# Optimization experiments

Measured on AMD Instinct MI355X. Metric: run time of the kernel, lower is better.

## Reference

```python
import jax, jax.numpy as jnp
import numpy as np

N, IN_DIM, OUT_DIM, NUM_HOPS, SD = 8192, 256, 256, 4, 64
ETA, LAM_LAP, LAM_SP, EPS = 0.5, 0.3, 0.05, 0.5
LN_EPS = 1e-5


def setup_inputs() -> dict:
    key = jax.random.key(0)
    ks = jax.random.split(key, 6)
    K = NUM_HOPS + 1
    return {
        "H": jax.random.normal(ks[0], (N, IN_DIM), jnp.float32),
        "hops": jax.random.normal(ks[1], (K, N, IN_DIM), jnp.float32),
        "L": jax.random.normal(ks[2], (N, N), jnp.float32),
        "U": jax.random.normal(ks[3], (K, IN_DIM, SD), jnp.float32) * 0.1,
        "W_in": jax.random.normal(ks[4], (OUT_DIM, IN_DIM), jnp.float32) * 0.05,
        "ln_gamma": jnp.ones((OUT_DIM,), jnp.float32),
        "ln_beta": jnp.zeros((OUT_DIM,), jnp.float32),
        "log_tau": jnp.zeros((), jnp.float32),
    }


def _per_hop(U_k, H_k):
    n = H_k.shape[0]
    Q, _ = jnp.linalg.qr(U_k)                 # [in_dim, sd]
    Z = Q.T @ H_k.T                           # [sd, n]
    G = Z @ Z.T                               # [sd, sd] Gram, reused
    Sigma = G / (n + 1e-8)
    tr_S = jnp.trace(Sigma)
    tr_S2 = jnp.sum(Sigma * Sigma)            # trace(Sigma @ Sigma), Sigma symmetric
    rank_eff = tr_S ** 2 / (tr_S2 + 1e-8)
    coeff = SD / (n * EPS ** 2 + 1e-8)
    M = jnp.eye(SD, dtype=Z.dtype) + coeff * G
    Lc = jnp.linalg.cholesky(M)
    MiZ = jax.scipy.linalg.cho_solve((Lc, True), Z)  # [sd, n]
    grad_R = (Q @ MiZ).T                      # [n, in_dim]
    return rank_eff, grad_R


def reference(H, hops, L, U, W_in, ln_gamma, ln_beta, log_tau):
    tau = jnp.clip(jnp.exp(log_tau), 0.1, 10.0)
    rank_effs, grads_R = jax.vmap(_per_hop)(U, hops)      # [K], [K,n,in_dim]
    lap_terms = jnp.einsum('nm,kmd->knd', L, hops)        # [K,n,in_dim]
    w = jax.nn.softmax(rank_effs / tau)                   # [K]
    grad_sum = jnp.einsum('k,knd->nd', w, grads_R)
    lap_sum = jnp.einsum('k,knd->nd', w, lap_terms)
    H_half = H + ETA * grad_sum - ETA * LAM_LAP * lap_sum
    H_prox = jnp.sign(H_half) * jax.nn.relu(jnp.abs(H_half) - LAM_SP * ETA)
    H_out = H_prox @ W_in.T
    mu = jnp.mean(H_out, axis=-1, keepdims=True)
    var = jnp.var(H_out, axis=-1, keepdims=True)
    H_out = (H_out - mu) * jax.lax.rsqrt(var + LN_EPS) * ln_gamma + ln_beta
    return H_out, rank_effs, w
```

## Files before the change

### kernel.cpp

```cpp
#include <hip/hip_runtime.h>
#include <stdint.h>


typedef __attribute__((ext_vector_type(8))) short  s16x8;
typedef __attribute__((ext_vector_type(4))) float  f32x4;

#define NNODE 8192
#define DIN   256
#define KHOP  5
#define SDM   64

static const size_t OFF_Q    = 0;
static const size_t OFF_QT   = OFF_Q   + (size_t)5*256*64*4;
static const size_t OFF_ZT   = OFF_QT  + (size_t)5*64*256*2;
static const size_t OFF_GP   = OFF_ZT  + (size_t)5*8192*64*2;
static const size_t OFF_LM   = OFF_GP  + (size_t)5*16*4096*4;
static const size_t OFF_RD   = OFF_LM  + (size_t)5*4096*4;
static const size_t OFF_LU   = OFF_RD  + (size_t)5*64*4;
static const size_t OFF_RDU  = OFF_LU  + (size_t)5*4096*4;
static const size_t OFF_RE   = OFF_RDU + (size_t)5*64*4;
static const size_t OFF_W    = OFF_RE  + 64;
static const size_t OFF_T2   = OFF_W   + 64;
static const size_t OFF_HWT  = OFF_T2  + (size_t)5*256*64*2;
static const size_t OFF_WBF  = OFF_HWT + (size_t)256*8192*2;
static const size_t OFF_HP   = OFF_WBF + (size_t)256*256*2;
static const size_t OFF_PART = OFF_HP  + (size_t)8192*256*2;
static const size_t OFF_LBF  = OFF_PART + (size_t)9*8192*256*2;

__device__ __forceinline__ unsigned short f2bf(float f){
  unsigned u = __builtin_bit_cast(unsigned, f);
  u += 0x7FFFu + ((u >> 16) & 1u);
  return (unsigned short)(u >> 16);
}
__device__ __forceinline__ float bf2f(unsigned h){
  return __builtin_bit_cast(float, h << 16);
}
__device__ __forceinline__ void gl_lds16(const void* g, void* l){
  __builtin_amdgcn_global_load_lds(
      (const __attribute__((address_space(1))) void*)g,
      (__attribute__((address_space(3))) void*)l, 16, 0, 0);
}
__device__ __forceinline__ f32x4 mfma16(s16x8 a, s16x8 b, f32x4 c){
  return __builtin_amdgcn_mfma_f32_16x16x32_bf16(a, b, c, 0, 0, 0);
}

__device__ void chol64(float* A, float* rd, int tid){
  #pragma unroll 1
  for (int j = 0; j < 64; ++j){
    if (tid == 0){
      float d = sqrtf(fmaxf(A[j*65+j], 1e-20f));
      A[j*65+j] = d; rd[j] = 1.0f / d;
    }
    __syncthreads();
    float rinv = rd[j];
    for (int i = j+1+tid; i < 64; i += 256) A[i*65+j] *= rinv;
    __syncthreads();
    #pragma unroll 1
    for (int e = tid; e < 4096; e += 256){
      int i = e >> 6, l = e & 63;
      if (i > j && l > j && l <= i) A[i*65+l] -= A[i*65+j] * A[l*65+j];
    }
    __syncthreads();
  }
}

__global__ __launch_bounds__(256) void k_pre(const float* __restrict__ U,
                                             const float* __restrict__ L,
                                             float* __restrict__ Lu,
                                             float* __restrict__ rdu,
                                             unsigned short* __restrict__ Lbf){
  __shared__ float A[64*65];
  __shared__ float rd[64];
  int tid = threadIdx.x;
  if (blockIdx.x >= 5){
    size_t e = ((size_t)(blockIdx.x-5)*256 + tid)*8;
    f32x4 a = *(const f32x4*)(L + e);
    f32x4 b = *(const f32x4*)(L + e + 4);
    uint4 u;
    u.x = (unsigned)f2bf(a[0]) | ((unsigned)f2bf(a[1]) << 16);
    u.y = (unsigned)f2bf(a[2]) | ((unsigned)f2bf(a[3]) << 16);
    u.z = (unsigned)f2bf(b[0]) | ((unsigned)f2bf(b[1]) << 16);
    u.w = (unsigned)f2bf(b[2]) | ((unsigned)f2bf(b[3]) << 16);
    *(uint4*)(Lbf + e) = u;
    return;
  }
  int k = blockIdx.x;
  const float* Uk = U + (size_t)k*16384;
  int ti = tid >> 4, tj = tid & 15;
  float s[16];
  #pragma unroll
  for (int i = 0; i < 16; ++i) s[i] = 0.0f;
  for (int n = 0; n < 256; ++n){
    f32x4 xa = *(const f32x4*)(Uk + n*64 + ti*4);
    f32x4 xb = *(const f32x4*)(Uk + n*64 + tj*4);
    #pragma unroll
    for (int p = 0; p < 4; ++p)
      #pragma unroll
      for (int q = 0; q < 4; ++q) s[p*4+q] += xa[p]*xb[q];
  }
  #pragma unroll
  for (int p = 0; p < 4; ++p)
    #pragma unroll
    for (int q = 0; q < 4; ++q) A[(ti*4+p)*65 + tj*4+q] = s[p*4+q];
  __syncthreads();
  chol64(A, rd, tid);
  for (int e = tid; e < 4096; e += 256) Lu[(size_t)k*4096 + e] = A[(e>>6)*65 + (e&63)];
  if (tid < 64) rdu[k*64 + tid] = rd[tid];
}

__global__ __launch_bounds__(256) void k_qsolve(const float* __restrict__ U,
                                                const float* __restrict__ Lu,
                                                const float* __restrict__ rdu,
                                                float* __restrict__ Qf,
                                                unsigned short* __restrict__ Qt){
  int k = blockIdx.y, tid = threadIdx.x, wave = tid >> 6, lane = tid & 63;
  __shared__ float Al[64*65];
  __shared__ float rds[64];
  for (int e = tid; e < 4096; e += 256) Al[(e>>6)*65 + (e&63)] = Lu[(size_t)k*4096 + e];
  if (tid < 64) rds[tid] = rdu[k*64 + tid];
  __syncthreads();
  int n = blockIdx.x*4 + wave;
  float x = U[((size_t)k*256 + n)*64 + lane];
  #pragma unroll
  for (int j = 0; j < 64; ++j){
    float zj = __shfl(x, j) * rds[j];
    x = (lane == j) ? zj : (lane > j ? x - Al[lane*65+j]*zj : x);
  }
  Qf[((size_t)k*256 + n)*64 + lane] = x;
  Qt[(size_t)k*16384 + lane*256 + n] = f2bf(x);
}

__global__ __launch_bounds__(256,2) void k_zgemm(const float* __restrict__ hops,
                                                 const unsigned short* __restrict__ Qt,
                                                 unsigned short* __restrict__ Zt){
  __shared__ __align__(16) unsigned short Al[128][72];
  __shared__ __align__(16) unsigned short Bl[64][64];
  int tid = threadIdx.x, lane = tid & 63, wave = tid >> 6;
  int q = lane >> 4, r = lane & 15;
  int k = blockIdx.y, m0 = blockIdx.x * 128;
  f32x4 acc[2][4];
  #pragma unroll
  for (int a = 0; a < 2; ++a)
    #pragma unroll
    for (int b = 0; b < 4; ++b) acc[a][b] = (f32x4){0,0,0,0};
  int rr = tid >> 1, half = tid & 1;
  for (int it = 0; it < 4; ++it){
    __syncthreads();
    #pragma unroll
    for (int i = 0; i < 2; ++i){
      int o = i*4096 + wave*1024 + lane*16;
      int srow = o >> 7, kc = (o & 127) >> 1;
      gl_lds16(Qt + (size_t)k*16384 + srow*256 + it*64 + kc,
               (char*)&Bl[0][0] + i*4096 + wave*1024);
    }
    const float* ga = hops + ((size_t)k*NNODE + m0 + rr)*256 + it*64 + half*32;
    f32x4 v[8];
    #pragma unroll
    for (int i = 0; i < 8; ++i) v[i] = *(const f32x4*)(ga + i*4);
    #pragma unroll
    for (int i = 0; i < 4; ++i){
      s16x8 t;
      #pragma unroll
      for (int j = 0; j < 8; ++j){ int e = i*8+j; t[j] = (short)f2bf(v[e>>2][e&3]); }
      *(s16x8*)&Al[rr][half*32 + i*8] = t;
    }
    __syncthreads();
    #pragma unroll
    for (int h = 0; h < 2; ++h){
      int ko = h*32 + q*8;
      s16x8 b[4];
      #pragma unroll
      for (int ni = 0; ni < 4; ++ni) b[ni] = *(const s16x8*)&Bl[ni*16 + r][ko];
      #pragma unroll
      for (int mi = 0; mi < 2; ++mi){
        s16x8 a = *(const s16x8*)&Al[wave*32 + mi*16 + r][ko];
        #pragma unroll
        for (int ni = 0; ni < 4; ++ni) acc[mi][ni] = mfma16(a, b[ni], acc[mi][ni]);
      }
    }
  }
  #pragma unroll
  for (int mi = 0; mi < 2; ++mi)
    #pragma unroll
    for (int ni = 0; ni < 4; ++ni)
      #pragma unroll
      for (int ii = 0; ii < 4; ++ii){
        int m = m0 + wave*32 + mi*16 + q*4 + ii;
        int sc = ni*16 + r;
        Zt[((size_t)k*NNODE + m)*64 + sc] = f2bf(acc[mi][ni][ii]);
      }
}

__global__ __launch_bounds__(256) void k_gpart(const unsigned short* __restrict__ Zt,
                                               float* __restrict__ Gp){
  int k = blockIdx.x, c = blockIdx.y, tid = threadIdx.x;
  __shared__ __align__(16) unsigned short Zl[128][64];
  int ti = tid >> 4, tj = tid & 15;
  float acc[16];
  #pragma unroll
  for (int i = 0; i < 16; ++i) acc[i] = 0.0f;
  for (int sub = 0; sub < 4; ++sub){
    const char* gb = (const char*)Zt + ((size_t)k*NNODE + c*512 + sub*128)*128;
    __syncthreads();
    #pragma unroll
    for (int i = 0; i < 4; ++i){
      int o = i*4096 + tid*16;
      *(uint4*)((char*)&Zl[0][0] + o) = *(const uint4*)(gb + o);
    }
    __syncthreads();
    for (int n = 0; n < 128; ++n){
      const unsigned short* row = &Zl[n][0];
      uint2 ua = *(const uint2*)(row + ti*4);
      uint2 ub = *(const uint2*)(row + tj*4);
      float xa[4] = { bf2f(ua.x & 0xffff), bf2f(ua.x >> 16), bf2f(ua.y & 0xffff), bf2f(ua.y >> 16) };
      float xb[4] = { bf2f(ub.x & 0xffff), bf2f(ub.x >> 16), bf2f(ub.y & 0xffff), bf2f(ub.y >> 16) };
      #pragma unroll
      for (int p = 0; p < 4; ++p)
        #pragma unroll
        for (int qn = 0; qn < 4; ++qn) acc[p*4+qn] += xa[p]*xb[qn];
    }
  }
  float* o = Gp + ((size_t)k*16 + c)*4096;
  #pragma unroll
  for (int p = 0; p < 4; ++p)
    #pragma unroll
    for (int qn = 0; qn < 4; ++qn) o[(ti*4+p)*64 + tj*4+qn] = acc[p*4+qn];
}

__global__ __launch_bounds__(256) void k_gred(const float* __restrict__ Gp,
                                              float* __restrict__ LmO,
                                              float* __restrict__ rdO,
                                              float* __restrict__ reO){
  int k = blockIdx.x, tid = threadIdx.x;
  __shared__ float A[64*65];
  __shared__ float rd[64];
  __shared__ float red[256];
  int ti = tid >> 4, tj = tid & 15;
  float s[16];
  #pragma unroll
  for (int i = 0; i < 16; ++i) s[i] = 0.0f;
  for (int c = 0; c < 16; ++c){
    const float* g = Gp + ((size_t)k*16 + c)*4096 + (ti*4)*64 + tj*4;
    #pragma unroll
    for (int p = 0; p < 4; ++p)
      #pragma unroll
      for (int qn = 0; qn < 4; ++qn) s[p*4+qn] += g[p*64+qn];
  }
  const float sc    = 1.0f / (8192.0f + 1e-8f);
  const float coeff = 64.0f / (8192.0f*0.25f + 1e-8f);
  float trp = 0.0f, tr2p = 0.0f;
  #pragma unroll
  for (int p = 0; p < 4; ++p)
    #pragma unroll
    for (int qn = 0; qn < 4; ++qn){
      float gg = s[p*4+qn];
      float sg = gg * sc;
      tr2p += sg*sg;
      int row = ti*4+p, col = tj*4+qn;
      if (row == col) trp += sg;
      A[row*65 + col] = (row == col ? 1.0f : 0.0f) + coeff*gg;
    }
  red[tid] = trp; __syncthreads();
  for (int o = 128; o > 0; o >>= 1){ if (tid < o) red[tid] += red[tid+o]; __syncthreads(); }
  float tr = red[0]; __syncthreads();
  red[tid] = tr2p; __syncthreads();
  for (int o = 128; o > 0; o >>= 1){ if (tid < o) red[tid] += red[tid+o]; __syncthreads(); }
  float tr2 = red[0]; __syncthreads();
  if (tid == 0) reO[k] = tr*tr / (tr2 + 1e-8f);
  chol64(A, rd, tid);
  for (int e = tid; e < 4096; e += 256) LmO[(size_t)k*4096 + e] = A[(e>>6)*65 + (e&63)];
  if (tid < 64) rdO[k*64 + tid] = rd[tid];
}

__global__ void k_soft(const float* __restrict__ re, const float* __restrict__ ltau,
                       float* __restrict__ wv, float* __restrict__ dtail){
  if (threadIdx.x == 0){
    float tau = expf(ltau[0]);
    tau = fminf(fmaxf(tau, 0.1f), 10.0f);
    float r[5], m = -1e30f;
    for (int i = 0; i < 5; ++i){ r[i] = re[i]; m = fmaxf(m, r[i]); }
    float e[5], sum = 0.0f;
    for (int i = 0; i < 5; ++i){ e[i] = expf((r[i]-m)/tau); sum += e[i]; }
    for (int i = 0; i < 5; ++i){
      float w = e[i]/sum;
      wv[i] = w; dtail[i] = r[i]; dtail[5+i] = w;
    }
  }
}

__global__ __launch_bounds__(256) void k_post(const float* __restrict__ hops,
                                              const float* __restrict__ wv,
                                              unsigned short* __restrict__ hwT,
                                              const float* __restrict__ Qf,
                                              const float* __restrict__ LmI,
                                              const float* __restrict__ rdI,
                                              unsigned short* __restrict__ T2w,
                                              const float* __restrict__ Win,
                                              unsigned short* __restrict__ Wbf){
  __shared__ float T[64*65];
  __shared__ float rds[64];
  int bid = blockIdx.x, tid = threadIdx.x;
  if (bid < 512){
    int n0 = (bid & 127)*64, d0 = (bid >> 7)*64;
    float wl[5];
    #pragma unroll
    for (int k = 0; k < 5; ++k) wl[k] = -0.15f * wv[k];
    for (int e = tid; e < 1024; e += 256){
      int row = e >> 4, c4 = (e & 15)*4;
      f32x4 acc = (f32x4){0,0,0,0};
      #pragma unroll
      for (int k = 0; k < 5; ++k){
        f32x4 v = *(const f32x4*)(hops + ((size_t)k*NNODE + n0 + row)*256 + d0 + c4);
        acc += v * wl[k];
      }
      T[row*65 + c4+0] = acc[0]; T[row*65 + c4+1] = acc[1];
      T[row*65 + c4+2] = acc[2]; T[row*65 + c4+3] = acc[3];
    }
    __syncthreads();
    for (int e = tid; e < 1024; e += 256){
      int dr = e >> 4, c4 = (e & 15)*4;
      unsigned short h0 = f2bf(T[(c4+0)*65 + dr]);
      unsigned short h1 = f2bf(T[(c4+1)*65 + dr]);
      unsigned short h2 = f2bf(T[(c4+2)*65 + dr]);
      unsigned short h3 = f2bf(T[(c4+3)*65 + dr]);
      uint2 u; u.x = (unsigned)h0 | ((unsigned)h1 << 16); u.y = (unsigned)h2 | ((unsigned)h3 << 16);
      *(uint2*)(hwT + (size_t)(d0+dr)*NNODE + n0 + c4) = u;
    }
  } else if (bid < 832){
    int i = bid - 512;
    int k = i >> 6, xb = i & 63;
    int wave = tid >> 6, lane = tid & 63;
    for (int e = tid; e < 4096; e += 256) T[(e>>6)*65 + (e&63)] = LmI[(size_t)k*4096 + e];
    if (tid < 64) rds[tid] = rdI[k*64 + tid];
    __syncthreads();
    int n = xb*4 + wave;
    float x = Qf[((size_t)k*256 + n)*64 + lane];
    #pragma unroll
    for (int j = 0; j < 64; ++j){
      float zj = __shfl(x, j) * rds[j];
      x = (lane == j) ? zj : (lane > j ? x - T[lane*65+j]*zj : x);
    }
    #pragma unroll
    for (int j = 63; j >= 0; --j){
      float yj = __shfl(x, j) * rds[j];
      x = (lane == j) ? yj : (lane < j ? x - T[j*65+lane]*yj : x);
    }
    float scale = 0.5f * wv[k];
    T2w[((size_t)k*256 + n)*64 + lane] = f2bf(scale * x);
  } else {
    int i = bid - 832;
    int e = (i*256 + tid)*4;
    f32x4 v = *(const f32x4*)(Win + e);
    uint2 u;
    u.x = (unsigned)f2bf(v[0]) | ((unsigned)f2bf(v[1]) << 16);
    u.y = (unsigned)f2bf(v[2]) | ((unsigned)f2bf(v[3]) << 16);
    *(uint2*)(Wbf + e) = u;
  }
}

__global__ __launch_bounds__(256,2) void k_gg(const unsigned short* __restrict__ Lbf,
                                              const unsigned short* __restrict__ Bt,
                                              unsigned short* __restrict__ part,
                                              const unsigned short* __restrict__ Zt,
                                              const unsigned short* __restrict__ T2w){
  __shared__ __align__(16) unsigned short SM[24960];
  int bid = blockIdx.x, tid = threadIdx.x;
  int lane = tid & 63, wave = tid >> 6;
  int q = lane >> 4, r = lane & 15;
  if (bid < 512){
    unsigned short* Al = SM;
    unsigned short* Bl = SM + 16*520;
    int m0 = (bid & 63) * 128;
    int by = bid >> 6;
    size_t kbase = (size_t)by * 1024;
    int sr = lane >> 3, sc8 = (lane & 7) * 8;
    f32x4 acc[8][4];
    #pragma unroll
    for (int a = 0; a < 8; ++a)
      #pragma unroll
      for (int b = 0; b < 4; ++b) acc[a][b] = (f32x4){0,0,0,0};
    for (int it = 0; it < 16; ++it){
      size_t k0 = kbase + it*64;
      __syncthreads();
      #pragma unroll
      for (int i = 0; i < 12; ++i){
        int c = i*4 + wave;
        if (c < 16){
          gl_lds16(Lbf + (size_t)(m0 + c*8 + sr)*NNODE + k0 + sc8,
                   (char*)Al + c*1040 + lane*16);
        } else {
          int cb = c - 16;
          gl_lds16(Bt + (size_t)(cb*8 + sr)*NNODE + k0 + sc8,
                   (char*)Bl + cb*1040 + lane*16);
        }
      }
      __syncthreads();
      #pragma unroll
      for (int h = 0; h < 2; ++h){
        int ko = h*32 + q*8;
        s16x8 b[4];
        #pragma unroll
        for (int ni = 0; ni < 4; ++ni){
          int d = wave*64 + ni*16 + r;
          b[ni] = *(const s16x8*)(Bl + (d>>3)*520 + (d&7)*64 + ko);
        }
        #pragma unroll
        for (int mi = 0; mi < 8; ++mi){
          int m = mi*16 + r;
          s16x8 a = *(const s16x8*)(Al + (m>>3)*520 + (m&7)*64 + ko);
          #pragma unroll
          for (int ni = 0; ni < 4; ++ni) acc[mi][ni] = mfma16(a, b[ni], acc[mi][ni]);
        }
      }
    }
    unsigned short* o = part + (size_t)by * 2097152;
    #pragma unroll
    for (int mi = 0; mi < 8; ++mi)
      #pragma unroll
      for (int ni = 0; ni < 4; ++ni)
        #pragma unroll
        for (int ii = 0; ii < 4; ++ii){
          int m = m0 + mi*16 + q*4 + ii;
          int n = wave*64 + ni*16 + r;
          o[(size_t)m*256 + n] = f2bf(acc[mi][ni][ii]);
        }
  } else {
    unsigned short* Al = SM;
    unsigned short* Bl = SM + 2048;
    int m0 = (bid - 512) * 32;
    f32x4 acc[2][4];
    #pragma unroll
    for (int a = 0; a < 2; ++a)
      #pragma unroll
      for (int b = 0; b < 4; ++b) acc[a][b] = (f32x4){0,0,0,0};
    for (int kk = 0; kk < 5; ++kk){
      __syncthreads();
      {
        int o = wave*1024 + lane*16;
        gl_lds16((const char*)Zt + ((size_t)kk*NNODE + m0)*128 + o,
                 (char*)Al + wave*1024);
      }
      #pragma unroll
      for (int i = 0; i < 8; ++i){
        int o = i*4096 + wave*1024 + lane*16;
        gl_lds16((const char*)T2w + (size_t)kk*32768 + o,
                 (char*)Bl + i*4096 + wave*1024);
      }
      __syncthreads();
      #pragma unroll
      for (int h = 0; h < 2; ++h){
        int ko = h*32 + q*8;
        s16x8 b[4];
        #pragma unroll
        for (int ni = 0; ni < 4; ++ni) b[ni] = *(const s16x8*)&Bl[(wave*64 + ni*16 + r)*64 + ko];
        #pragma unroll
        for (int mi = 0; mi < 2; ++mi){
          s16x8 a = *(const s16x8*)&Al[(mi*16 + r)*64 + ko];
          #pragma unroll
          for (int ni = 0; ni < 4; ++ni) acc[mi][ni] = mfma16(a, b[ni], acc[mi][ni]);
        }
      }
    }
    unsigned short* o8 = part + (size_t)8 * 2097152;
    #pragma unroll
    for (int mi = 0; mi < 2; ++mi)
      #pragma unroll
      for (int ni = 0; ni < 4; ++ni)
        #pragma unroll
        for (int ii = 0; ii < 4; ++ii){
          int m = m0 + mi*16 + q*4 + ii;
          int n = wave*64 + ni*16 + r;
          o8[(size_t)m*256 + n] = f2bf(acc[mi][ni][ii]);
        }
  }
}

__global__ __launch_bounds__(256) void k_combine(const float* __restrict__ H,
                                                 const unsigned short* __restrict__ part,
                                                 unsigned short* __restrict__ Hp){
  size_t e = ((size_t)blockIdx.x*256 + threadIdx.x)*4;
  f32x4 h = *(const f32x4*)(H + e);
  float s0 = h[0], s1 = h[1], s2 = h[2], s3 = h[3];
  #pragma unroll
  for (int sl = 0; sl < 9; ++sl){
    uint2 u = *(const uint2*)(part + (size_t)sl*2097152 + e);
    s0 += bf2f(u.x & 0xffff); s1 += bf2f(u.x >> 16);
    s2 += bf2f(u.y & 0xffff); s3 += bf2f(u.y >> 16);
  }
  #define PROX(a) ({ float _t = fabsf(a) - 0.025f; _t > 0.0f ? copysignf(_t,(a)) : 0.0f; })
  uint2 o;
  o.x = (unsigned)f2bf(PROX(s0)) | ((unsigned)f2bf(PROX(s1)) << 16);
  o.y = (unsigned)f2bf(PROX(s2)) | ((unsigned)f2bf(PROX(s3)) << 16);
  *(uint2*)(Hp + e) = o;
}

__global__ __launch_bounds__(256,2) void k_finln(const unsigned short* __restrict__ Hp,
                                                 const unsigned short* __restrict__ Wbf,
                                                 const float* __restrict__ gamma,
                                                 const float* __restrict__ beta,
                                                 float* __restrict__ out){
  __shared__ __align__(16) unsigned short Al[64][64];
  __shared__ __align__(16) unsigned short Bl[256][64];
  __shared__ float SmR[64][4];
  __shared__ float SqR[64][4];
  int tid = threadIdx.x, lane = tid & 63, wave = tid >> 6;
  int q = lane >> 4, r = lane & 15;
  int m0 = blockIdx.x * 64;
  f32x4 acc[4][4];
  #pragma unroll
  for (int a = 0; a < 4; ++a)
    #pragma unroll
    for (int b = 0; b < 4; ++b) acc[a][b] = (f32x4){0,0,0,0};
  for (int it = 0; it < 4; ++it){
    __syncthreads();
    #pragma unroll
    for (int i = 0; i < 2; ++i){
      int o = i*4096 + wave*1024 + lane*16;
      int row = o >> 7, kc = o & 127;
      gl_lds16((const char*)Hp + (size_t)(m0+row)*512 + it*128 + kc,
               (char*)&Al[0][0] + i*4096 + wave*1024);
    }
    #pragma unroll
    for (int i = 0; i < 8; ++i){
      int o = i*4096 + wave*1024 + lane*16;
      int n = o >> 7, kc = o & 127;
      gl_lds16((const char*)Wbf + (size_t)n*512 + it*128 + kc,
               (char*)&Bl[0][0] + i*4096 + wave*1024);
    }
    __syncthreads();
    #pragma unroll
    for (int h = 0; h < 2; ++h){
      int ko = h*32 + q*8;
      s16x8 b[4];
      #pragma unroll
      for (int ni = 0; ni < 4; ++ni) b[ni] = *(const s16x8*)&Bl[wave*64 + ni*16 + r][ko];
      #pragma unroll
      for (int mi = 0; mi < 4; ++mi){
        s16x8 a = *(const s16x8*)&Al[mi*16 + r][ko];
        #pragma unroll
        for (int ni = 0; ni < 4; ++ni) acc[mi][ni] = mfma16(a, b[ni], acc[mi][ni]);
      }
    }
  }
  #pragma unroll
  for (int mi = 0; mi < 4; ++mi)
    #pragma unroll
    for (int ii = 0; ii < 4; ++ii){
      float sm = 0.0f, sq = 0.0f;
      #pragma unroll
      for (int ni = 0; ni < 4; ++ni){
        float v = acc[mi][ni][ii];
        sm += v; sq += v*v;
      }
      #pragma unroll
      for (int o = 1; o < 16; o <<= 1){ sm += __shfl_xor(sm, o, 64); sq += __shfl_xor(sq, o, 64); }
      if (r == 0){
        int rl = mi*16 + q*4 + ii;
        SmR[rl][wave] = sm; SqR[rl][wave] = sq;
      }
    }
  __syncthreads();
  float g[4], b[4];
  #pragma unroll
  for (int ni = 0; ni < 4; ++ni){
    g[ni] = gamma[wave*64 + ni*16 + r];
    b[ni] = beta [wave*64 + ni*16 + r];
  }
  #pragma unroll
  for (int mi = 0; mi < 4; ++mi)
    #pragma unroll
    for (int ii = 0; ii < 4; ++ii){
      int rl = mi*16 + q*4 + ii;
      float sm = SmR[rl][0] + SmR[rl][1] + SmR[rl][2] + SmR[rl][3];
      float sq = SqR[rl][0] + SqR[rl][1] + SqR[rl][2] + SqR[rl][3];
      float mean = sm * (1.0f/256.0f);
      float var  = sq * (1.0f/256.0f) - mean*mean;
      float rs   = rsqrtf(var + 1e-5f);
      #pragma unroll
      for (int ni = 0; ni < 4; ++ni){
        out[(size_t)(m0+rl)*256 + wave*64 + ni*16 + r] =
            (acc[mi][ni][ii] - mean)*rs*g[ni] + b[ni];
      }
    }
}

extern "C" void kernel_launch(void* const* d_in, const int* in_sizes, int n_in,
                              void* d_out, int out_size, void* d_ws, size_t ws_size,
                              hipStream_t stream){
  const float* H    = (const float*)d_in[0];
  const float* hops = (const float*)d_in[1];
  const float* Lmat = (const float*)d_in[2];
  const float* U    = (const float*)d_in[3];
  const float* Win  = (const float*)d_in[4];
  const float* gam  = (const float*)d_in[5];
  const float* bet  = (const float*)d_in[6];
  const float* ltau = (const float*)d_in[7];
  float* out = (float*)d_out;

  char* ws = (char*)d_ws;
  float*          Qf   = (float*)(ws + OFF_Q);
  unsigned short* Qt   = (unsigned short*)(ws + OFF_QT);
  unsigned short* Zt   = (unsigned short*)(ws + OFF_ZT);
  float*          Gp   = (float*)(ws + OFF_GP);
  float*          Lm   = (float*)(ws + OFF_LM);
  float*          rdw  = (float*)(ws + OFF_RD);
  float*          Lu   = (float*)(ws + OFF_LU);
  float*          rdu  = (float*)(ws + OFF_RDU);
  float*          re   = (float*)(ws + OFF_RE);
  float*          wv   = (float*)(ws + OFF_W);
  unsigned short* T2w  = (unsigned short*)(ws + OFF_T2);
  unsigned short* hwT  = (unsigned short*)(ws + OFF_HWT);
  unsigned short* Wbf  = (unsigned short*)(ws + OFF_WBF);
  unsigned short* Hp   = (unsigned short*)(ws + OFF_HP);
  unsigned short* part = (unsigned short*)(ws + OFF_PART);
  unsigned short* Lbf  = (unsigned short*)(ws + OFF_LBF);

  hipLaunchKernelGGL(k_pre,    dim3(32773),  dim3(256), 0, stream, U, Lmat, Lu, rdu, Lbf);
  hipLaunchKernelGGL(k_qsolve, dim3(64,5),   dim3(256), 0, stream, U, Lu, rdu, Qf, Qt);
  hipLaunchKernelGGL(k_zgemm,  dim3(64,5),   dim3(256), 0, stream, hops, Qt, Zt);
  hipLaunchKernelGGL(k_gpart,  dim3(5,16),   dim3(256), 0, stream, Zt, Gp);
  hipLaunchKernelGGL(k_gred,   dim3(5),      dim3(256), 0, stream, Gp, Lm, rdw, re);
  hipLaunchKernelGGL(k_soft,   dim3(1),      dim3(64),  0, stream, re, ltau, wv, out + 2097152);
  hipLaunchKernelGGL(k_post,   dim3(896),    dim3(256), 0, stream, hops, wv, hwT, Qf, Lm, rdw, T2w, Win, Wbf);
  hipLaunchKernelGGL(k_gg,     dim3(768),    dim3(256), 0, stream, Lbf, hwT, part, Zt, T2w);
  hipLaunchKernelGGL(k_combine,dim3(2048),   dim3(256), 0, stream, H, part, Hp);
  hipLaunchKernelGGL(k_finln,  dim3(128),    dim3(256), 0, stream, Hp, Wbf, gam, bet, out);
}
```

Before: 752.9 us.

## Replace block-wide Cholesky with single-wave register/shuffle version; grid-stride L conversion

The 64x64 Cholesky used in k_pre and k_gred is rewritten so that one wavefront holds one matrix row per lane in registers and broadcasts pivot values with shuffles. This removes the three __syncthreads per column of the old 256-thread LDS version. The L-to-bf16 conversion in k_pre now loops 16 times per block, cutting the grid from about 32K blocks to about 2K. Costs: a 64-float register array per lane with fully unrolled loops (register pressure and code size), the other three waves sit idle during the factorization, and the store pattern changes to row-per-lane.

New measurement: 628.1 us. -16.6%, faster.

```diff
diff --git a/kernel.cpp b/kernel.cpp
--- a/kernel.cpp
+++ b/kernel.cpp
@@ -44,23 +44,19 @@
   return __builtin_amdgcn_mfma_f32_16x16x32_bf16(a, b, c, 0, 0, 0);
 }
 
-__device__ void chol64(float* A, float* rd, int tid){
-  #pragma unroll 1
+__device__ __forceinline__ void wave_chol64(float* a, float& rdk, int lane){
+  rdk = 0.0f;
+  #pragma unroll
   for (int j = 0; j < 64; ++j){
-    if (tid == 0){
-      float d = sqrtf(fmaxf(A[j*65+j], 1e-20f));
-      A[j*65+j] = d; rd[j] = 1.0f / d;
-    }
-    __syncthreads();
-    float rinv = rd[j];
-    for (int i = j+1+tid; i < 64; i += 256) A[i*65+j] *= rinv;
-    __syncthreads();
-    #pragma unroll 1
-    for (int e = tid; e < 4096; e += 256){
-      int i = e >> 6, l = e & 63;
-      if (i > j && l > j && l <= i) A[i*65+l] -= A[i*65+j] * A[l*65+j];
-    }
-    __syncthreads();
+    float dj  = __shfl(a[j], j);
+    float d   = sqrtf(fmaxf(dj, 1e-20f));
+    float rdj = 1.0f / d;
+    float cj  = a[j] * rdj;
+    a[j] = cj;
+    if (lane == j) rdk = rdj;
+    #pragma unroll
+    for (int l = j+1; l < 64; ++l)
+      a[l] -= cj * __shfl(cj, l);
   }
 }
 
@@ -70,18 +66,21 @@
                                              float* __restrict__ rdu,
                                              unsigned short* __restrict__ Lbf){
   __shared__ float A[64*65];
-  __shared__ float rd[64];
   int tid = threadIdx.x;
   if (blockIdx.x >= 5){
-    size_t e = ((size_t)(blockIdx.x-5)*256 + tid)*8;
-    f32x4 a = *(const f32x4*)(L + e);
-    f32x4 b = *(const f32x4*)(L + e + 4);
-    uint4 u;
-    u.x = (unsigned)f2bf(a[0]) | ((unsigned)f2bf(a[1]) << 16);
-    u.y = (unsigned)f2bf(a[2]) | ((unsigned)f2bf(a[3]) << 16);
-    u.z = (unsigned)f2bf(b[0]) | ((unsigned)f2bf(b[1]) << 16);
-    u.w = (unsigned)f2bf(b[2]) | ((unsigned)f2bf(b[3]) << 16);
-    *(uint4*)(Lbf + e) = u;
+    size_t base = (size_t)(blockIdx.x - 5);
+    #pragma unroll 4
+    for (int it = 0; it < 16; ++it){
+      size_t e = ((base + (size_t)it*2048)*256 + tid)*8;
+      f32x4 a = *(const f32x4*)(L + e);
+      f32x4 b = *(const f32x4*)(L + e + 4);
+      uint4 u;
+      u.x = (unsigned)f2bf(a[0]) | ((unsigned)f2bf(a[1]) << 16);
+      u.y = (unsigned)f2bf(a[2]) | ((unsigned)f2bf(a[3]) << 16);
+      u.z = (unsigned)f2bf(b[0]) | ((unsigned)f2bf(b[1]) << 16);
+      u.w = (unsigned)f2bf(b[2]) | ((unsigned)f2bf(b[3]) << 16);
+      *(uint4*)(Lbf + e) = u;
+    }
     return;
   }
   int k = blockIdx.x;
@@ -103,9 +102,17 @@
     #pragma unroll
     for (int q = 0; q < 4; ++q) A[(ti*4+p)*65 + tj*4+q] = s[p*4+q];
   __syncthreads();
-  chol64(A, rd, tid);
-  for (int e = tid; e < 4096; e += 256) Lu[(size_t)k*4096 + e] = A[(e>>6)*65 + (e&63)];
-  if (tid < 64) rdu[k*64 + tid] = rd[tid];
+  if (tid < 64){
+    int lane = tid;
+    float a[64];
+    #pragma unroll
+    for (int l = 0; l < 64; ++l) a[l] = A[lane*65 + l];
+    float rdk;
+    wave_chol64(a, rdk, lane);
+    #pragma unroll
+    for (int l = 0; l < 64; ++l) Lu[(size_t)k*4096 + lane*64 + l] = a[l];
+    rdu[k*64 + lane] = rdk;
+  }
 }
 
 __global__ __launch_bounds__(256) void k_qsolve(const float* __restrict__ U,
@@ -233,7 +240,6 @@
                                               float* __restrict__ reO){
   int k = blockIdx.x, tid = threadIdx.x;
   __shared__ float A[64*65];
-  __shared__ float rd[64];
   __shared__ float red[256];
   int ti = tid >> 4, tj = tid & 15;
   float s[16];
@@ -265,11 +271,20 @@
   float tr = red[0]; __syncthreads();
   red[tid] = tr2p; __syncthreads();
   for (int o = 128; o > 0; o >>= 1){ if (tid < o) red[tid] += red[tid+o]; __syncthreads(); }
-  float tr2 = red[0]; __syncthreads();
+  float tr2 = red[0];
   if (tid == 0) reO[k] = tr*tr / (tr2 + 1e-8f);
-  chol64(A, rd, tid);
-  for (int e = tid; e < 4096; e += 256) LmO[(size_t)k*4096 + e] = A[(e>>6)*65 + (e&63)];
-  if (tid < 64) rdO[k*64 + tid] = rd[tid];
+  __syncthreads();
+  if (tid < 64){
+    int lane = tid;
+    float a[64];
+    #pragma unroll
+    for (int l = 0; l < 64; ++l) a[l] = A[lane*65 + l];
+    float rdk;
+    wave_chol64(a, rdk, lane);
+    #pragma unroll
+    for (int l = 0; l < 64; ++l) LmO[(size_t)k*4096 + lane*64 + l] = a[l];
+    rdO[k*64 + lane] = rdk;
+  }
 }
 
 __global__ void k_soft(const float* __restrict__ re, const float* __restrict__ ltau,
@@ -615,7 +630,7 @@
   unsigned short* part = (unsigned short*)(ws + OFF_PART);
   unsigned short* Lbf  = (unsigned short*)(ws + OFF_LBF);
 
-  hipLaunchKernelGGL(k_pre,    dim3(32773),  dim3(256), 0, stream, U, Lmat, Lu, rdu, Lbf);
+  hipLaunchKernelGGL(k_pre,    dim3(2053),   dim3(256), 0, stream, U, Lmat, Lu, rdu, Lbf);
   hipLaunchKernelGGL(k_qsolve, dim3(64,5),   dim3(256), 0, stream, U, Lu, rdu, Qf, Qt);
   hipLaunchKernelGGL(k_zgemm,  dim3(64,5),   dim3(256), 0, stream, hops, Qt, Zt);
   hipLaunchKernelGGL(k_gpart,  dim3(5,16),   dim3(256), 0, stream, Zt, Gp);
```
